# Optimization experiments

Measured on AMD Instinct MI355X. Metric: run time of the kernel, lower is better.

The kernel has to match this reference:

```python
import jax, jax.numpy as jnp
import numpy as np

DIM = 1024
NUM_HEADS = 16
HEAD_DIM = DIM // NUM_HEADS
SCALE = HEAD_DIM ** -0.5


def setup_inputs() -> dict:
    key = jax.random.key(0)
    k1, k2, k3 = jax.random.split(key, 3)
    B, N = 2, 2048
    x = jax.random.normal(k1, (B, N, DIM), dtype=jnp.float32)
    W_qkv = jax.random.normal(k2, (DIM, 3 * DIM), dtype=jnp.float32) * (DIM ** -0.5)
    b_qkv = jnp.zeros((3 * DIM,), dtype=jnp.float32)
    W_proj = jax.random.normal(k3, (DIM, DIM), dtype=jnp.float32) * (DIM ** -0.5)
    b_proj = jnp.zeros((DIM,), dtype=jnp.float32)
    return {"x": x, "W_qkv": W_qkv, "b_qkv": b_qkv, "W_proj": W_proj, "b_proj": b_proj}


def reference(x, W_qkv, b_qkv, W_proj, b_proj):
    B, N, D = x.shape
    qkv = x @ W_qkv + b_qkv                      # [B, N, 3D]
    qkv = qkv.reshape(B, N, 3, NUM_HEADS, HEAD_DIM)
    qkv = jnp.transpose(qkv, (2, 0, 3, 1, 4))    # [3, B, H, N, hd]
    q, k, v = qkv[0], qkv[1], qkv[2]
    attn = jnp.einsum('bhqd,bhkd->bhqk', q, k) * SCALE  # [B, H, N, N]
    attn = jax.nn.softmax(attn, axis=-1)
    out = jnp.einsum('bhqk,bhkd->bhqd', attn, v)        # [B, H, N, hd]
    out = jnp.transpose(out, (0, 2, 1, 3)).reshape(B, N, D)
    out = out @ W_proj + b_proj
    return out
```

## Files before the change

kernel.cpp:

```cpp
#include <hip/hip_runtime.h>


typedef __bf16 bf16_t;
typedef __bf16 bf16x2 __attribute__((ext_vector_type(2)));
typedef __bf16 bf16x4 __attribute__((ext_vector_type(4)));
typedef __bf16 bf16x8 __attribute__((ext_vector_type(8)));
typedef float  f32x4  __attribute__((ext_vector_type(4)));

#define NTOK 2048
#define DIM  1024
#define NH   16
#define HD   64
#define SCL2 0.18033688011112042f

#define MFMA16(a, b, c) __builtin_amdgcn_mfma_f32_16x16x32_bf16((a), (b), (c), 0, 0, 0)

__device__ __forceinline__ void gload_lds16(const void* g, void* l) {
  __builtin_amdgcn_global_load_lds((const __attribute__((address_space(1))) void*)g,
                                   (__attribute__((address_space(3))) void*)l, 16, 0, 0);
}

__device__ __forceinline__ void transpose_cvt_tile(const float* __restrict__ W,
                                                   bf16_t* __restrict__ WT,
                                                   int rows, int cols, int bx, int by) {
  __shared__ float tile[32][33];
  int j0 = bx * 32, i0 = by * 32;
  int c = threadIdx.x & 31, r0 = threadIdx.x >> 5;
#pragma unroll
  for (int it = 0; it < 4; ++it) {
    int r = r0 + it * 8;
    tile[r][c] = W[(long)(i0 + r) * cols + j0 + c];
  }
  __syncthreads();
#pragma unroll
  for (int it = 0; it < 4; ++it) {
    int r = r0 + it * 8;
    WT[(long)(j0 + r) * rows + i0 + c] = (bf16_t)tile[c][r];
  }
}

__global__ __launch_bounds__(256) void k_prep(const float* __restrict__ x,
                                              bf16_t* __restrict__ xb,
                                              const float* __restrict__ Wq,
                                              bf16_t* __restrict__ WqT,
                                              const float* __restrict__ Wp,
                                              bf16_t* __restrict__ WpT) {
  int id = blockIdx.x;
  if (id < 2048) {
    int i = (id * 256 + threadIdx.x) * 8;
    float4 a = *(const float4*)(x + i);
    float4 b = *(const float4*)(x + i + 4);
    bf16x8 v;
    v[0] = (bf16_t)a.x; v[1] = (bf16_t)a.y; v[2] = (bf16_t)a.z; v[3] = (bf16_t)a.w;
    v[4] = (bf16_t)b.x; v[5] = (bf16_t)b.y; v[6] = (bf16_t)b.z; v[7] = (bf16_t)b.w;
    *(bf16x8*)(xb + i) = v;
  } else if (id < 2048 + 3072) {
    int t = id - 2048;
    transpose_cvt_tile(Wq, WqT, 1024, 3072, t % 96, t / 96);
  } else {
    int t = id - 5120;
    transpose_cvt_tile(Wp, WpT, 1024, 1024, t & 31, t >> 5);
  }
}

__device__ __forceinline__ void gemm_core(const bf16_t* __restrict__ A,
                                          const bf16_t* __restrict__ B,
                                          int K, int bm, int bn,
                                          bf16_t* As, bf16_t* Bs, f32x4 acc[4][4]) {
  const int t = threadIdx.x;
  const int lane = t & 63;
  const int w = t >> 6;
  const int wr = (w >> 1) * 64, wc = (w & 1) * 64;
  const int l15 = lane & 15, g = lane >> 4;
  const int srow = t >> 2, scol = (t & 3) * 8;
  const f32x4 vzero = {0.f, 0.f, 0.f, 0.f};
#pragma unroll
  for (int m = 0; m < 4; ++m)
#pragma unroll
    for (int n = 0; n < 4; ++n) acc[m][n] = vzero;

  const bf16_t* ga = A + (long)(bm + srow) * K + scol;
  const bf16_t* gb = B + (long)(bn + srow) * K + scol;
  bf16_t* lA = As + srow * 32 + scol;
  bf16_t* lB = Bs + srow * 32 + scol;
  const long rstep = 64l * K;

  for (int k0 = 0; k0 < K; k0 += 32) {
    gload_lds16(ga + k0,         lA);
    gload_lds16(ga + rstep + k0, lA + 64 * 32);
    gload_lds16(gb + k0,         lB);
    gload_lds16(gb + rstep + k0, lB + 64 * 32);
    __syncthreads();
    bf16x8 af[4], bfv[4];
#pragma unroll
    for (int m = 0; m < 4; ++m)
      af[m] = *(const bf16x8*)(As + (wr + m * 16 + l15) * 32 + g * 8);
#pragma unroll
    for (int n = 0; n < 4; ++n)
      bfv[n] = *(const bf16x8*)(Bs + (wc + n * 16 + l15) * 32 + g * 8);
#pragma unroll
    for (int m = 0; m < 4; ++m)
#pragma unroll
      for (int n = 0; n < 4; ++n)
        acc[m][n] = MFMA16(af[m], bfv[n], acc[m][n]);
    __syncthreads();
  }
}

__global__ __launch_bounds__(256) void k_gemm_qkv(const bf16_t* __restrict__ xb,
                                                  const bf16_t* __restrict__ WqT,
                                                  const float* __restrict__ bq,
                                                  bf16_t* __restrict__ Qb,
                                                  bf16_t* __restrict__ Kb,
                                                  bf16_t* __restrict__ Vt) {
  __shared__ alignas(16) bf16_t As[128 * 32];
  __shared__ alignas(16) bf16_t Bs[128 * 32];
  f32x4 acc[4][4];
  const int bm = blockIdx.y * 128, bn = blockIdx.x * 128;
  gemm_core(xb, WqT, DIM, bm, bn, As, Bs, acc);

  const int lane = threadIdx.x & 63, w = threadIdx.x >> 6;
  const int wr = (w >> 1) * 64, wc = (w & 1) * 64;
  const int l15 = lane & 15, g = lane >> 4;
#pragma unroll
  for (int n = 0; n < 4; ++n) {
    int col = bn + wc + n * 16 + l15;
    float bias = bq[col];
    int t3 = col >> 10, rem = col & 1023;
    int h = rem >> 6, d = rem & 63;
#pragma unroll
    for (int m = 0; m < 4; ++m) {
      int rowb = bm + wr + m * 16 + g * 4;
#pragma unroll
      for (int r = 0; r < 4; ++r) {
        int row = rowb + r;
        int b = row >> 11, tok = row & 2047;
        int bh = b * NH + h;
        float val = acc[m][n][r] + bias;
        if (t3 == 0) {
          Qb[bh * (NTOK * HD) + tok * HD + d] = (bf16_t)(val * SCL2);
        } else if (t3 == 1) {
          int rr = tok & 63;
          int off = bh * (NTOK * HD) + (tok >> 6) * 4096 + rr * 64 +
                    (((d >> 3) ^ (rr & 7)) << 3) + (d & 7);
          Kb[off] = (bf16_t)val;
        } else {
          int ct = tok & 63;
          int off = bh * (NTOK * HD) + (tok >> 6) * 4096 + d * 64 +
                    (((ct >> 3) ^ (d & 7)) << 3) + (ct & 7);
          Vt[off] = (bf16_t)val;
        }
      }
    }
  }
}

__global__ __launch_bounds__(256, 3) void k_attn(const bf16_t* __restrict__ Qb,
                                                 const bf16_t* __restrict__ Kb,
                                                 const bf16_t* __restrict__ Vt,
                                                 bf16_t* __restrict__ Ob) {
  __shared__ alignas(16) bf16_t Ks[2][64 * 64];
  __shared__ alignas(16) bf16_t Vs[2][64 * 64];
  __shared__ alignas(16) char  P2[4][4096];

  const int b0 = blockIdx.x;
  const int swz = (b0 & 7) * 64 + (b0 >> 3);
  const int qt = swz & 15, bh = swz >> 4;
  const int b = bh >> 4, h = bh & 15;
  const int t = threadIdx.x;
  const int w = t >> 6, lane = t & 63;
  const int l15 = lane & 15, g = lane >> 4;
  const bf16_t* Qp = Qb + bh * (NTOK * HD);
  const bf16_t* Kp = Kb + bh * (NTOK * HD);
  const bf16_t* Vp = Vt + bh * (NTOK * HD);
  const int q0 = qt * 128 + w * 32;
  char* P2w = &P2[w][0];

  const int cs0 = ((g ^ (l15 & 7)) << 4);
  const int cs1 = cs0 ^ 64;

  bf16x8 qfr[2][2];
#pragma unroll
  for (int qf = 0; qf < 2; ++qf)
#pragma unroll
    for (int kk = 0; kk < 2; ++kk)
      qfr[qf][kk] = *(const bf16x8*)(Qp + (q0 + qf * 16 + l15) * HD + kk * 32 + g * 8);

  bf16x8 ones;
#pragma unroll
  for (int i = 0; i < 8; ++i) ones[i] = (bf16_t)1.0f;

  const f32x4 vzero = {0.f, 0.f, 0.f, 0.f};
  f32x4 o[2][4];
#pragma unroll
  for (int qf = 0; qf < 2; ++qf)
#pragma unroll
    for (int df = 0; df < 4; ++df) o[qf][df] = vzero;
  f32x4 o_sum[2] = {vzero, vzero};

  auto stage = [&](int buf, int tile) {
    const bf16_t* gk = Kp + tile * 4096 + t * 8;
    const bf16_t* gv = Vp + tile * 4096 + t * 8;
    gload_lds16(gk,        (char*)Ks[buf] + t * 16);
    gload_lds16(gk + 2048, (char*)Ks[buf] + 4096 + t * 16);
    gload_lds16(gv,        (char*)Vs[buf] + t * 16);
    gload_lds16(gv + 2048, (char*)Vs[buf] + 4096 + t * 16);
  };

  stage(0, 0);
  __syncthreads();
  int cur = 0;

  for (int kt = 0; kt < NTOK; kt += 64) {
    if (kt + 64 < NTOK) stage(cur ^ 1, (kt >> 6) + 1);
    const char* kbuf = (const char*)Ks[cur];
    const char* vbuf = (const char*)Vs[cur];
    f32x4 s[2][4];
    __builtin_amdgcn_s_setprio(1);
#pragma unroll
    for (int kf = 0; kf < 4; ++kf) {
      int rb = (kf * 16 + l15) * 128;
      bf16x8 ka0 = *(const bf16x8*)(kbuf + rb + cs0);
      bf16x8 ka1 = *(const bf16x8*)(kbuf + rb + cs1);
      s[0][kf] = MFMA16(ka0, qfr[0][0], vzero);
      s[1][kf] = MFMA16(ka0, qfr[1][0], vzero);
      s[0][kf] = MFMA16(ka1, qfr[0][1], s[0][kf]);
      s[1][kf] = MFMA16(ka1, qfr[1][1], s[1][kf]);
    }
    __builtin_amdgcn_s_setprio(0);
#pragma unroll
    for (int qf = 0; qf < 2; ++qf)
#pragma unroll
      for (int kf = 0; kf < 4; ++kf) {
        bf16x4 pw;
        pw[0] = (bf16_t)__builtin_amdgcn_exp2f(s[qf][kf][0]);
        pw[1] = (bf16_t)__builtin_amdgcn_exp2f(s[qf][kf][1]);
        pw[2] = (bf16_t)__builtin_amdgcn_exp2f(s[qf][kf][2]);
        pw[3] = (bf16_t)__builtin_amdgcn_exp2f(s[qf][kf][3]);
        *(bf16x4*)(P2w + qf * 2048 + (2 * kf + (g >> 1)) * 256 + l15 * 16 + 8 * (g & 1)) = pw;
      }
    __builtin_amdgcn_s_setprio(1);
#pragma unroll
    for (int kb = 0; kb < 2; ++kb) {
      bf16x8 pf0 = *(const bf16x8*)(P2w + kb * 1024 + lane * 16);
      bf16x8 pf1 = *(const bf16x8*)(P2w + 2048 + kb * 1024 + lane * 16);
      int csk = kb ? cs1 : cs0;
      o_sum[0] = MFMA16(ones, pf0, o_sum[0]);
      o_sum[1] = MFMA16(ones, pf1, o_sum[1]);
#pragma unroll
      for (int df = 0; df < 4; ++df) {
        bf16x8 va = *(const bf16x8*)(vbuf + (df * 16 + l15) * 128 + csk);
        o[0][df] = MFMA16(va, pf0, o[0][df]);
        o[1][df] = MFMA16(va, pf1, o[1][df]);
      }
    }
    __builtin_amdgcn_s_setprio(0);
    __syncthreads();
    cur ^= 1;
  }
#pragma unroll
  for (int qf = 0; qf < 2; ++qf) {
    float inv = 1.0f / o_sum[qf][0];
    int tok = q0 + qf * 16 + l15;
    bf16_t* op = Ob + (long)(b * NTOK + tok) * DIM + h * HD;
#pragma unroll
    for (int df = 0; df < 4; ++df) {
#pragma unroll
      for (int rp = 0; rp < 2; ++rp) {
        bf16x2 v2;
        v2[0] = (bf16_t)(o[qf][df][rp * 2]     * inv);
        v2[1] = (bf16_t)(o[qf][df][rp * 2 + 1] * inv);
        *(bf16x2*)(op + df * 16 + g * 4 + rp * 2) = v2;
      }
    }
  }
}

__global__ __launch_bounds__(256) void k_gemm_proj(const bf16_t* __restrict__ Ob,
                                                   const bf16_t* __restrict__ WpT,
                                                   const float* __restrict__ bp,
                                                   float* __restrict__ out) {
  __shared__ alignas(16) bf16_t As[128 * 32];
  __shared__ alignas(16) bf16_t Bs[128 * 32];
  f32x4 acc[4][4];
  const int bm = blockIdx.y * 128, bn = blockIdx.x * 128;
  gemm_core(Ob, WpT, DIM, bm, bn, As, Bs, acc);

  const int lane = threadIdx.x & 63, w = threadIdx.x >> 6;
  const int wr = (w >> 1) * 64, wc = (w & 1) * 64;
  const int l15 = lane & 15, g = lane >> 4;
#pragma unroll
  for (int n = 0; n < 4; ++n) {
    int col = bn + wc + n * 16 + l15;
    float bias = bp[col];
#pragma unroll
    for (int m = 0; m < 4; ++m) {
      int rowb = bm + wr + m * 16 + g * 4;
#pragma unroll
      for (int r = 0; r < 4; ++r)
        out[(long)(rowb + r) * DIM + col] = acc[m][n][r] + bias;
    }
  }
}

extern "C" void kernel_launch(void* const* d_in, const int* in_sizes, int n_in,
                              void* d_out, int out_size, void* d_ws, size_t ws_size,
                              hipStream_t stream) {
  const float* x     = (const float*)d_in[0];
  const float* Wqkv  = (const float*)d_in[1];
  const float* bqkv  = (const float*)d_in[2];
  const float* Wproj = (const float*)d_in[3];
  const float* bproj = (const float*)d_in[4];
  float* out = (float*)d_out;

  char* ws = (char*)d_ws;
  bf16_t* xb  = (bf16_t*)(ws);
  bf16_t* WqT = (bf16_t*)(ws + (8l  << 20));
  bf16_t* WpT = (bf16_t*)(ws + (14l << 20));
  bf16_t* Qb  = (bf16_t*)(ws + (16l << 20));
  bf16_t* Kb  = (bf16_t*)(ws + (24l << 20));
  bf16_t* Vt  = (bf16_t*)(ws + (32l << 20));
  bf16_t* Ob  = (bf16_t*)(ws);

  k_prep<<<6144, 256, 0, stream>>>(x, xb, Wqkv, WqT, Wproj, WpT);
  k_gemm_qkv<<<dim3(24, 32), 256, 0, stream>>>(xb, WqT, bqkv, Qb, Kb, Vt);
  k_attn<<<512, 256, 0, stream>>>(Qb, Kb, Vt, Ob);
  k_gemm_proj<<<dim3(8, 32), 256, 0, stream>>>(Ob, WpT, bproj, out);
}
```

Baseline: 120.0 us.

## Split attention KV range across wave pairs and remap GEMM block indices per XCD

The attention kernel now has each wave cover 64 queries instead of 32. Waves 0-1 and waves 2-3 each process half of the key/value sequence using separate double-buffered LDS tiles, and their partial outputs and row sums are combined through LDS at the end. This reuses each loaded K/V fragment across more query fragments and interleaves the S computation, exp and PV per half-tile. The cost is more registers (occupancy bound lowered from 3 to 2) and an extra reduction step. The QKV and projection GEMMs switch to a 1D grid with a block mapping meant to keep column tiles on the same XCD for L2 locality.

```diff
diff --git a/kernel.cpp b/kernel.cpp
--- a/kernel.cpp
+++ b/kernel.cpp
@@ -116,7 +116,10 @@
   __shared__ alignas(16) bf16_t As[128 * 32];
   __shared__ alignas(16) bf16_t Bs[128 * 32];
   f32x4 acc[4][4];
-  const int bm = blockIdx.y * 128, bn = blockIdx.x * 128;
+  const int bid = blockIdx.x;
+  const int xcd = bid & 7, ib = bid >> 3;
+  const int bn = (xcd * 3 + (ib >> 5)) * 128;
+  const int bm = (ib & 31) * 128;
   gemm_core(xb, WqT, DIM, bm, bn, As, Bs, acc);
 
   const int lane = threadIdx.x & 63, w = threadIdx.x >> 6;
@@ -155,12 +158,12 @@
   }
 }
 
-__global__ __launch_bounds__(256, 3) void k_attn(const bf16_t* __restrict__ Qb,
+__global__ __launch_bounds__(256, 2) void k_attn(const bf16_t* __restrict__ Qb,
                                                  const bf16_t* __restrict__ Kb,
                                                  const bf16_t* __restrict__ Vt,
                                                  bf16_t* __restrict__ Ob) {
-  __shared__ alignas(16) bf16_t Ks[2][64 * 64];
-  __shared__ alignas(16) bf16_t Vs[2][64 * 64];
+  __shared__ alignas(16) bf16_t Ks[2][2][4096];
+  __shared__ alignas(16) bf16_t Vs[2][2][4096];
   __shared__ alignas(16) char  P2[4][4096];
 
   const int b0 = blockIdx.x;
@@ -170,18 +173,19 @@
   const int t = threadIdx.x;
   const int w = t >> 6, lane = t & 63;
   const int l15 = lane & 15, g = lane >> 4;
+  const int qh = w & 1, p = w >> 1;
   const bf16_t* Qp = Qb + bh * (NTOK * HD);
   const bf16_t* Kp = Kb + bh * (NTOK * HD);
   const bf16_t* Vp = Vt + bh * (NTOK * HD);
-  const int q0 = qt * 128 + w * 32;
+  const int q0 = qt * 128 + qh * 64;
   char* P2w = &P2[w][0];
 
   const int cs0 = ((g ^ (l15 & 7)) << 4);
   const int cs1 = cs0 ^ 64;
 
-  bf16x8 qfr[2][2];
-#pragma unroll
-  for (int qf = 0; qf < 2; ++qf)
+  bf16x8 qfr[4][2];
+#pragma unroll
+  for (int qf = 0; qf < 4; ++qf)
 #pragma unroll
     for (int kk = 0; kk < 2; ++kk)
       qfr[qf][kk] = *(const bf16x8*)(Qp + (q0 + qf * 16 + l15) * HD + kk * 32 + g * 8);
@@ -191,86 +195,103 @@
   for (int i = 0; i < 8; ++i) ones[i] = (bf16_t)1.0f;
 
   const f32x4 vzero = {0.f, 0.f, 0.f, 0.f};
-  f32x4 o[2][4];
-#pragma unroll
-  for (int qf = 0; qf < 2; ++qf)
+  f32x4 o[4][4];
+#pragma unroll
+  for (int qf = 0; qf < 4; ++qf)
 #pragma unroll
     for (int df = 0; df < 4; ++df) o[qf][df] = vzero;
-  f32x4 o_sum[2] = {vzero, vzero};
-
+  f32x4 o_sum[4] = {vzero, vzero, vzero, vzero};
+
+  const int tt = t & 127;
   auto stage = [&](int buf, int tile) {
-    const bf16_t* gk = Kp + tile * 4096 + t * 8;
-    const bf16_t* gv = Vp + tile * 4096 + t * 8;
-    gload_lds16(gk,        (char*)Ks[buf] + t * 16);
-    gload_lds16(gk + 2048, (char*)Ks[buf] + 4096 + t * 16);
-    gload_lds16(gv,        (char*)Vs[buf] + t * 16);
-    gload_lds16(gv + 2048, (char*)Vs[buf] + 4096 + t * 16);
+    const bf16_t* gk = Kp + tile * 4096 + tt * 8;
+    const bf16_t* gv = Vp + tile * 4096 + tt * 8;
+#pragma unroll
+    for (int j = 0; j < 4; ++j) {
+      gload_lds16(gk + j * 1024, (char*)Ks[p][buf] + tt * 16 + j * 2048);
+      gload_lds16(gv + j * 1024, (char*)Vs[p][buf] + tt * 16 + j * 2048);
+    }
   };
 
-  stage(0, 0);
+  stage(0, p * 16);
   __syncthreads();
   int cur = 0;
 
-  for (int kt = 0; kt < NTOK; kt += 64) {
-    if (kt + 64 < NTOK) stage(cur ^ 1, (kt >> 6) + 1);
-    const char* kbuf = (const char*)Ks[cur];
-    const char* vbuf = (const char*)Vs[cur];
-    f32x4 s[2][4];
-    __builtin_amdgcn_s_setprio(1);
-#pragma unroll
-    for (int kf = 0; kf < 4; ++kf) {
-      int rb = (kf * 16 + l15) * 128;
-      bf16x8 ka0 = *(const bf16x8*)(kbuf + rb + cs0);
-      bf16x8 ka1 = *(const bf16x8*)(kbuf + rb + cs1);
-      s[0][kf] = MFMA16(ka0, qfr[0][0], vzero);
-      s[1][kf] = MFMA16(ka0, qfr[1][0], vzero);
-      s[0][kf] = MFMA16(ka1, qfr[0][1], s[0][kf]);
-      s[1][kf] = MFMA16(ka1, qfr[1][1], s[1][kf]);
-    }
-    __builtin_amdgcn_s_setprio(0);
-#pragma unroll
-    for (int qf = 0; qf < 2; ++qf)
-#pragma unroll
-      for (int kf = 0; kf < 4; ++kf) {
-        bf16x4 pw;
-        pw[0] = (bf16_t)__builtin_amdgcn_exp2f(s[qf][kf][0]);
-        pw[1] = (bf16_t)__builtin_amdgcn_exp2f(s[qf][kf][1]);
-        pw[2] = (bf16_t)__builtin_amdgcn_exp2f(s[qf][kf][2]);
-        pw[3] = (bf16_t)__builtin_amdgcn_exp2f(s[qf][kf][3]);
-        *(bf16x4*)(P2w + qf * 2048 + (2 * kf + (g >> 1)) * 256 + l15 * 16 + 8 * (g & 1)) = pw;
+  for (int i = 0; i < 16; ++i) {
+    if (i < 15) stage(cur ^ 1, p * 16 + i + 1);
+    const char* kbuf = (const char*)Ks[p][cur];
+    const char* vbuf = (const char*)Vs[p][cur];
+#pragma unroll
+    for (int kb = 0; kb < 2; ++kb) {
+      __builtin_amdgcn_s_setprio(1);
+#pragma unroll
+      for (int kfh = 0; kfh < 2; ++kfh) {
+        int kf = kb * 2 + kfh;
+        int rb = (kf * 16 + l15) * 128;
+        bf16x8 ka0 = *(const bf16x8*)(kbuf + rb + cs0);
+        bf16x8 ka1 = *(const bf16x8*)(kbuf + rb + cs1);
+#pragma unroll
+        for (int qf = 0; qf < 4; ++qf) {
+          f32x4 s = MFMA16(ka0, qfr[qf][0], vzero);
+          s = MFMA16(ka1, qfr[qf][1], s);
+          bf16x4 pw;
+          pw[0] = (bf16_t)__builtin_amdgcn_exp2f(s[0]);
+          pw[1] = (bf16_t)__builtin_amdgcn_exp2f(s[1]);
+          pw[2] = (bf16_t)__builtin_amdgcn_exp2f(s[2]);
+          pw[3] = (bf16_t)__builtin_amdgcn_exp2f(s[3]);
+          *(bf16x4*)(P2w + qf * 1024 +
+                     ((kfh * 2 + (g >> 1)) * 16 + l15) * 16 + (g & 1) * 8) = pw;
+        }
       }
-    __builtin_amdgcn_s_setprio(1);
-#pragma unroll
-    for (int kb = 0; kb < 2; ++kb) {
-      bf16x8 pf0 = *(const bf16x8*)(P2w + kb * 1024 + lane * 16);
-      bf16x8 pf1 = *(const bf16x8*)(P2w + 2048 + kb * 1024 + lane * 16);
       int csk = kb ? cs1 : cs0;
-      o_sum[0] = MFMA16(ones, pf0, o_sum[0]);
-      o_sum[1] = MFMA16(ones, pf1, o_sum[1]);
-#pragma unroll
-      for (int df = 0; df < 4; ++df) {
-        bf16x8 va = *(const bf16x8*)(vbuf + (df * 16 + l15) * 128 + csk);
-        o[0][df] = MFMA16(va, pf0, o[0][df]);
-        o[1][df] = MFMA16(va, pf1, o[1][df]);
+      bf16x8 va[4];
+#pragma unroll
+      for (int df = 0; df < 4; ++df)
+        va[df] = *(const bf16x8*)(vbuf + (df * 16 + l15) * 128 + csk);
+#pragma unroll
+      for (int qf = 0; qf < 4; ++qf) {
+        bf16x8 pf = *(const bf16x8*)(P2w + qf * 1024 + lane * 16);
+        o_sum[qf] = MFMA16(ones, pf, o_sum[qf]);
+#pragma unroll
+        for (int df = 0; df < 4; ++df)
+          o[qf][df] = MFMA16(va[df], pf, o[qf][df]);
       }
-    }
-    __builtin_amdgcn_s_setprio(0);
+      __builtin_amdgcn_s_setprio(0);
+    }
     __syncthreads();
     cur ^= 1;
   }
-#pragma unroll
-  for (int qf = 0; qf < 2; ++qf) {
-    float inv = 1.0f / o_sum[qf][0];
-    int tok = q0 + qf * 16 + l15;
-    bf16_t* op = Ob + (long)(b * NTOK + tok) * DIM + h * HD;
-#pragma unroll
-    for (int df = 0; df < 4; ++df) {
-#pragma unroll
-      for (int rp = 0; rp < 2; ++rp) {
-        bf16x2 v2;
-        v2[0] = (bf16_t)(o[qf][df][rp * 2]     * inv);
-        v2[1] = (bf16_t)(o[qf][df][rp * 2 + 1] * inv);
-        *(bf16x2*)(op + df * 16 + g * 4 + rp * 2) = v2;
+
+  if (w >= 2) {
+    float* scr = (w == 2) ? (float*)&Ks[0][0][0] : (float*)&Vs[0][0][0];
+    float* mb = scr + lane * 68;
+#pragma unroll
+    for (int qf = 0; qf < 4; ++qf) {
+#pragma unroll
+      for (int df = 0; df < 4; ++df)
+        *(f32x4*)(mb + qf * 16 + df * 4) = o[qf][df];
+      mb[64 + qf] = o_sum[qf][0];
+    }
+  }
+  __syncthreads();
+  if (w < 2) {
+    const float* scr = (w == 0) ? (const float*)&Ks[0][0][0] : (const float*)&Vs[0][0][0];
+    const float* mb = scr + lane * 68;
+#pragma unroll
+    for (int qf = 0; qf < 4; ++qf) {
+      float inv = 1.0f / (o_sum[qf][0] + mb[64 + qf]);
+      int tok = q0 + qf * 16 + l15;
+      bf16_t* op = Ob + (long)(b * NTOK + tok) * DIM + h * HD;
+#pragma unroll
+      for (int df = 0; df < 4; ++df) {
+        f32x4 part = *(const f32x4*)(mb + qf * 16 + df * 4);
+#pragma unroll
+        for (int rp = 0; rp < 2; ++rp) {
+          bf16x2 v2;
+          v2[0] = (bf16_t)((o[qf][df][rp * 2]     + part[rp * 2])     * inv);
+          v2[1] = (bf16_t)((o[qf][df][rp * 2 + 1] + part[rp * 2 + 1]) * inv);
+          *(bf16x2*)(op + df * 16 + g * 4 + rp * 2) = v2;
+        }
       }
     }
   }
@@ -283,7 +304,9 @@
   __shared__ alignas(16) bf16_t As[128 * 32];
   __shared__ alignas(16) bf16_t Bs[128 * 32];
   f32x4 acc[4][4];
-  const int bm = blockIdx.y * 128, bn = blockIdx.x * 128;
+  const int bid = blockIdx.x;
+  const int bn = (bid & 7) * 128;
+  const int bm = (bid >> 3) * 128;
   gemm_core(Ob, WpT, DIM, bm, bn, As, Bs, acc);
 
   const int lane = threadIdx.x & 63, w = threadIdx.x >> 6;
@@ -323,7 +346,7 @@
   bf16_t* Ob  = (bf16_t*)(ws);
 
   k_prep<<<6144, 256, 0, stream>>>(x, xb, Wqkv, WqT, Wproj, WpT);
-  k_gemm_qkv<<<dim3(24, 32), 256, 0, stream>>>(xb, WqT, bqkv, Qb, Kb, Vt);
+  k_gemm_qkv<<<768, 256, 0, stream>>>(xb, WqT, bqkv, Qb, Kb, Vt);
   k_attn<<<512, 256, 0, stream>>>(Qb, Kb, Vt, Ob);
-  k_gemm_proj<<<dim3(8, 32), 256, 0, stream>>>(Ob, WpT, bproj, out);
-}
+  k_gemm_proj<<<256, 256, 0, stream>>>(Ob, WpT, bproj, out);
+}
```

After: 123.1 us. 1.03x slower.
